# Kernel optimization log

Hardware: AMD Instinct MI355X
Metric: run time of the kernel (lower is better)

The kernel has to match this reference:

```python
import jax, jax.numpy as jnp
import numpy as np

N_NODES = 150000       # original nodes
N_FRAG_NODES = 300000  # nodes duplicated across fragments
N_FRAGS = 30000        # number of fragments (segments of fragments_batch)
E = 1200000            # edges in combined fragment graph
D = 128                # nhid


def seg_mean(x, seg, num):
    s = jax.ops.segment_sum(x, seg, num_segments=num)
    c = jax.ops.segment_sum(jnp.ones((x.shape[0], 1), x.dtype), seg, num_segments=num)
    return s / jnp.maximum(c, 1.0)


def setup_inputs() -> dict:
    key = jax.random.key(0)
    ks = jax.random.split(key, 8)
    x = jax.random.normal(ks[0], (N_NODES, D), dtype=jnp.float32)
    mapper = jax.random.randint(ks[1], (N_FRAG_NODES,), 0, N_NODES)
    batch = jnp.sort(jax.random.randint(ks[2], (N_FRAG_NODES,), 0, N_FRAGS))
    edge_index = jax.random.randint(ks[3], (2, E), 0, N_FRAG_NODES)
    W_u = jax.random.normal(ks[4], (D, D), dtype=jnp.float32) * 0.05
    b_u = jnp.zeros((D,), dtype=jnp.float32)
    W_gcn = jax.random.normal(ks[5], (D, D), dtype=jnp.float32) * 0.05
    b_gcn = jnp.zeros((D,), dtype=jnp.float32)
    return {
        "x": x,
        "fragments_nodes_mapper": mapper,
        "fragments_batch": batch,
        "edge_index": edge_index,
        "W_u": W_u,
        "b_u": b_u,
        "W_gcn": W_gcn,
        "b_gcn": b_gcn,
        "i": 0,
    }


def gcn_conv(x, edge_index, W, b, n):
    # PyG GCNConv: add self loops, symmetric normalization D^-1/2 (A+I) D^-1/2, then linear.
    xw = x @ W  # [n, D]
    loops = jnp.arange(n, dtype=edge_index.dtype)
    row = jnp.concatenate([edge_index[0], loops])  # source
    col = jnp.concatenate([edge_index[1], loops])  # target (aggregation index)
    deg = jax.ops.segment_sum(jnp.ones(row.shape[0], x.dtype), col, num_segments=n)
    dinv = jnp.where(deg > 0, jax.lax.rsqrt(jnp.maximum(deg, 1.0)), 0.0)
    norm = dinv[row] * dinv[col]  # [E+n]
    msg = xw[row] * norm[:, None]
    out = jax.ops.segment_sum(msg, col, num_segments=n)
    return out + b


def reference(x, fragments_nodes_mapper, fragments_batch, edge_index, W_u, b_u, W_gcn, b_gcn, i):
    if i == 0:
        x = x[fragments_nodes_mapper]  # gather: [N_FRAG_NODES, D]
    # fragment-level mean pooling, broadcast back to fragment-nodes
    fragment = seg_mean(x, fragments_batch, N_FRAGS)[fragments_batch]
    # U[i-1]: MLP(nhid, nhid, nlayer=1, with_final_activation=True) -> Linear + ReLU
    x = x + jax.nn.relu(fragment @ W_u + b_u)
    # pool duplicated fragment-nodes back onto original nodes, then re-broadcast
    x = seg_mean(x, fragments_nodes_mapper, N_NODES)[fragments_nodes_mapper]
    # GCN over the combined fragment graph
    x = gcn_conv(x, edge_index, W_gcn, b_gcn, N_FRAG_NODES)
    fragment_x = seg_mean(x, fragments_batch, N_FRAGS)  # [N_FRAGS, D]
    return (fragment_x, x)
```

## Files before the change

### kernel.cpp

```cpp
#include <hip/hip_runtime.h>
#include <hip/hip_bf16.h>

#define N_NODES      150000
#define N_FRAG_NODES 300000
#define N_FRAGS      30000
#define NEDGE        1200000
#define NCNT         (N_NODES + N_FRAG_NODES)
#define D            128
#define DV           32
#define SCAN_TILE    1024

typedef __attribute__((ext_vector_type(8))) short short8;
typedef __attribute__((ext_vector_type(8))) unsigned short u16x8;
typedef __attribute__((ext_vector_type(4))) float f32x4;

__device__ __forceinline__ unsigned short f2bf(float f) {
    unsigned u = __float_as_uint(f);
    u = (u + 0x7FFFu + ((u >> 16) & 1u)) >> 16;
    return (unsigned short)u;
}
__device__ __forceinline__ float bf2f(unsigned short u) {
    return __uint_as_float((unsigned)u << 16);
}

__global__ void k_prep(const int* __restrict__ mapper, const int* __restrict__ batch,
                       const int* __restrict__ ecol, int* __restrict__ mcnt,
                       int* __restrict__ ccnt, int* __restrict__ startb) {
    int i = blockIdx.x * blockDim.x + threadIdx.x;
    if (i < NEDGE) atomicAdd(&ccnt[ecol[i]], 1);
    if (i < N_FRAG_NODES) atomicAdd(&mcnt[mapper[i]], 1);
    if (i <= N_FRAGS) {
        int lo = 0, hi = N_FRAG_NODES;
        while (lo < hi) { int mid = (lo + hi) >> 1; if (batch[mid] < i) lo = mid + 1; else hi = mid; }
        startb[i] = lo;
    }
}

__global__ void k_scan_tile(const int* __restrict__ cnt, int* __restrict__ combst,
                            int* __restrict__ tsum) {
    __shared__ int buf[SCAN_TILE];
    int tid = threadIdx.x;
    int i = blockIdx.x * SCAN_TILE + tid;
    int v = (i < NCNT) ? cnt[i] : 0;
    buf[tid] = v;
    __syncthreads();
    for (int off = 1; off < SCAN_TILE; off <<= 1) {
        int t = (tid >= off) ? buf[tid - off] : 0;
        __syncthreads();
        buf[tid] += t;
        __syncthreads();
    }
    if (i < NCNT) combst[i] = buf[tid] - v;
    if (tid == SCAN_TILE - 1) tsum[blockIdx.x] = buf[tid];
}

__global__ void k_scan_tsum(int* __restrict__ tsum, int ntiles,
                            int* __restrict__ mstart, int* __restrict__ cstart) {
    __shared__ int buf[SCAN_TILE];
    int tid = threadIdx.x;
    int v = (tid < ntiles) ? tsum[tid] : 0;
    buf[tid] = v;
    __syncthreads();
    for (int off = 1; off < SCAN_TILE; off <<= 1) {
        int t = (tid >= off) ? buf[tid - off] : 0;
        __syncthreads();
        buf[tid] += t;
        __syncthreads();
    }
    if (tid < ntiles) tsum[tid] = buf[tid] - v;
    if (tid == SCAN_TILE - 1) {
        mstart[N_NODES] = N_FRAG_NODES;
        cstart[N_FRAG_NODES] = buf[tid] - N_FRAG_NODES;
    }
}

__global__ void k_scan_add(const int* __restrict__ combst, const int* __restrict__ tsum,
                           int* __restrict__ mstart, int* __restrict__ cstart) {
    int i = blockIdx.x * blockDim.x + threadIdx.x;
    if (i >= NCNT) return;
    int v = combst[i] + tsum[i >> 10];
    if (i < N_NODES) mstart[i] = v;
    else cstart[i - N_NODES] = v - N_FRAG_NODES;
}

__global__ void k_frag_mean(const float4* __restrict__ x4, const int* __restrict__ mapper,
                            const int* __restrict__ startb, ushort4* __restrict__ frag16) {
    int g = threadIdx.x >> 5, lane = threadIdx.x & 31;
    int b = blockIdx.x * 8 + g;
    if (b >= N_FRAGS) return;
    int s = startb[b], e = startb[b + 1];
    float4 sA = {0.f, 0.f, 0.f, 0.f}, sB = {0.f, 0.f, 0.f, 0.f};
    int j = s;
    for (; j + 2 <= e; j += 2) {
        int m0 = mapper[j], m1 = mapper[j + 1];
        float4 v0 = x4[(size_t)m0 * DV + lane];
        float4 v1 = x4[(size_t)m1 * DV + lane];
        sA.x += v0.x; sA.y += v0.y; sA.z += v0.z; sA.w += v0.w;
        sB.x += v1.x; sB.y += v1.y; sB.z += v1.z; sB.w += v1.w;
    }
    if (j < e) {
        int m0 = mapper[j];
        float4 v0 = x4[(size_t)m0 * DV + lane];
        sA.x += v0.x; sA.y += v0.y; sA.z += v0.z; sA.w += v0.w;
    }
    float c = (float)(e - s); if (c < 1.f) c = 1.f;
    float inv = 1.f / c;
    ushort4 r = {f2bf((sA.x + sB.x) * inv), f2bf((sA.y + sB.y) * inv),
                 f2bf((sA.z + sB.z) * inv), f2bf((sA.w + sB.w) * inv)};
    frag16[(size_t)b * DV + lane] = r;
}

__global__ void k_build_wfrag(const float* __restrict__ W, short* __restrict__ wfrag) {
    int t = threadIdx.x;
    for (int e = t; e < 2048; e += 256) {
        int nt = e >> 8;
        int kk = (e >> 6) & 3;
        int lane = e & 63;
        int col = nt * 16 + (lane & 15);
        int kb = kk * 32 + ((lane >> 4) << 3);
        short8 v;
        #pragma unroll
        for (int j = 0; j < 8; ++j) v[j] = (short)f2bf(W[(kb + j) * D + col]);
        ((short8*)wfrag)[e] = v;
    }
}

template <bool RELU, bool BIAS>
__global__ void __launch_bounds__(256)
k_rowmat_mfma(const unsigned short* __restrict__ src16, const short* __restrict__ wfrag,
              const float* __restrict__ bias, unsigned short* __restrict__ dst16, int rows) {
    __shared__ short8 wl[2048];
    int tid = threadIdx.x;
    for (int e = tid; e < 2048; e += 256) wl[e] = ((const short8*)wfrag)[e];
    __syncthreads();
    int wv = tid >> 6, lane = tid & 63;
    int lrow = lane & 15;
    int lk8 = (lane >> 4);
    float bv[8];
    #pragma unroll
    for (int nt = 0; nt < 8; ++nt) bv[nt] = BIAS ? bias[nt * 16 + lrow] : 0.f;

    int chunk = blockIdx.x * 64;
    {
        int r = chunk + wv * 16 + lrow;
        short8 af[4];
        if (r < rows) {
            const short8* rowp = (const short8*)(src16 + (size_t)r * D);
            #pragma unroll
            for (int kk = 0; kk < 4; ++kk) af[kk] = rowp[kk * 4 + lk8];
        } else {
            #pragma unroll
            for (int kk = 0; kk < 4; ++kk) af[kk] = (short8)0;
        }
        f32x4 acc[8];
        #pragma unroll
        for (int nt = 0; nt < 8; ++nt) acc[nt] = (f32x4)0.f;
        #pragma unroll
        for (int nt = 0; nt < 8; ++nt) {
            #pragma unroll
            for (int kk = 0; kk < 4; ++kk)
                acc[nt] = __builtin_amdgcn_mfma_f32_16x16x32_bf16(
                              af[kk], wl[(nt * 4 + kk) * 64 + lane], acc[nt], 0, 0, 0);
        }
        int orow0 = chunk + wv * 16 + ((lane >> 4) << 2);
        #pragma unroll
        for (int nt = 0; nt < 8; ++nt) {
            int col = nt * 16 + lrow;
            #pragma unroll
            for (int reg = 0; reg < 4; ++reg) {
                int orow = orow0 + reg;
                if (orow < rows) {
                    float v = acc[nt][reg] + bv[nt];
                    if (RELU) v = fmaxf(v, 0.f);
                    dst16[(size_t)orow * D + col] = f2bf(v);
                }
            }
        }
    }
}

__global__ void k_fill_m(const int* __restrict__ mapper, const int* __restrict__ batch,
                         const int* __restrict__ mstart, int* __restrict__ mcnt,
                         int* __restrict__ mvals) {
    int i = blockIdx.x * blockDim.x + threadIdx.x;
    if (i >= N_FRAG_NODES) return;
    int k = mapper[i];
    int pos = atomicSub(&mcnt[k], 1) - 1;
    mvals[mstart[k] + pos] = batch[i];
}

__global__ void k_fill_e(const int* __restrict__ erow, const int* __restrict__ ecol,
                         const int* __restrict__ mapper, const int* __restrict__ cstart,
                         int* __restrict__ ccnt, int2* __restrict__ erecs) {
    int i = blockIdx.x * blockDim.x + threadIdx.x;
    if (i >= NEDGE) return;
    int c = ecol[i], r = erow[i];
    int pos = atomicSub(&ccnt[c], 1) - 1;
    float w = rsqrtf((float)(cstart[r + 1] - cstart[r] + 1));
    int2 rec;
    rec.x = mapper[r];
    rec.y = __float_as_int(w);
    erecs[cstart[c] + pos] = rec;
}

__global__ void k_pool_csr(const float4* __restrict__ x4, const u16x8* __restrict__ fragu8,
                           const int* __restrict__ mstart, const int* __restrict__ mvals,
                           u16x8* __restrict__ pooled8) {
    int g = threadIdx.x >> 4, lane = threadIdx.x & 15;
    int n = blockIdx.x * 16 + g;
    if (n >= N_NODES) return;
    int s = mstart[n], e = mstart[n + 1];
    u16x8 out = (u16x8)0;
    if (e > s) {
        float accA[8], accB[8];
        #pragma unroll
        for (int j = 0; j < 8; ++j) { accA[j] = 0.f; accB[j] = 0.f; }
        int t = s;
        for (; t + 2 <= e; t += 2) {
            int b0 = mvals[t], b1 = mvals[t + 1];
            u16x8 u0 = fragu8[(size_t)b0 * 16 + lane];
            u16x8 u1 = fragu8[(size_t)b1 * 16 + lane];
            #pragma unroll
            for (int j = 0; j < 8; ++j) {
                accA[j] += bf2f(u0[j]);
                accB[j] += bf2f(u1[j]);
            }
        }
        if (t < e) {
            int b0 = mvals[t];
            u16x8 u0 = fragu8[(size_t)b0 * 16 + lane];
            #pragma unroll
            for (int j = 0; j < 8; ++j) accA[j] += bf2f(u0[j]);
        }
        float inv = 1.f / (float)(e - s);
        float4 xv0 = x4[(size_t)n * DV + lane * 2];
        float4 xv1 = x4[(size_t)n * DV + lane * 2 + 1];
        out[0] = f2bf(fmaf(accA[0] + accB[0], inv, xv0.x));
        out[1] = f2bf(fmaf(accA[1] + accB[1], inv, xv0.y));
        out[2] = f2bf(fmaf(accA[2] + accB[2], inv, xv0.z));
        out[3] = f2bf(fmaf(accA[3] + accB[3], inv, xv0.w));
        out[4] = f2bf(fmaf(accA[4] + accB[4], inv, xv1.x));
        out[5] = f2bf(fmaf(accA[5] + accB[5], inv, xv1.y));
        out[6] = f2bf(fmaf(accA[6] + accB[6], inv, xv1.z));
        out[7] = f2bf(fmaf(accA[7] + accB[7], inv, xv1.w));
    }
    pooled8[(size_t)n * 16 + lane] = out;
}

__global__ void k_gcn_gather(const int* __restrict__ mapper, const int* __restrict__ cstart,
                             const int2* __restrict__ erecs, const u16x8* __restrict__ pw8,
                             const float* __restrict__ bgcn, float4* __restrict__ xout4) {
    int g = threadIdx.x >> 4, lane = threadIdx.x & 15;
    int c = blockIdx.x * 16 + g;
    if (c >= N_FRAG_NODES) return;
    int s = cstart[c], e = cstart[c + 1];
    float dc = rsqrtf((float)(e - s + 1));
    float accA[8], accB[8];
    #pragma unroll
    for (int j = 0; j < 8; ++j) { accA[j] = 0.f; accB[j] = 0.f; }
    int t = s;
    for (; t + 2 <= e; t += 2) {
        int2 r0 = erecs[t];
        int2 r1 = erecs[t + 1];
        u16x8 u0 = pw8[(size_t)r0.x * 16 + lane];
        u16x8 u1 = pw8[(size_t)r1.x * 16 + lane];
        float w0 = __int_as_float(r0.y);
        float w1 = __int_as_float(r1.y);
        #pragma unroll
        for (int j = 0; j < 8; ++j) {
            accA[j] = fmaf(bf2f(u0[j]), w0, accA[j]);
            accB[j] = fmaf(bf2f(u1[j]), w1, accB[j]);
        }
    }
    if (t < e) {
        int2 r0 = erecs[t];
        u16x8 u0 = pw8[(size_t)r0.x * 16 + lane];
        float w0 = __int_as_float(r0.y);
        #pragma unroll
        for (int j = 0; j < 8; ++j) accA[j] = fmaf(bf2f(u0[j]), w0, accA[j]);
    }
    u16x8 su = pw8[(size_t)mapper[c] * 16 + lane];
    float dc2 = dc * dc;
    const float4* bg4 = (const float4*)bgcn;
    float4 b0 = bg4[lane * 2], b1 = bg4[lane * 2 + 1];
    float4 o0, o1;
    o0.x = fmaf(accA[0] + accB[0], dc, fmaf(bf2f(su[0]), dc2, b0.x));
    o0.y = fmaf(accA[1] + accB[1], dc, fmaf(bf2f(su[1]), dc2, b0.y));
    o0.z = fmaf(accA[2] + accB[2], dc, fmaf(bf2f(su[2]), dc2, b0.z));
    o0.w = fmaf(accA[3] + accB[3], dc, fmaf(bf2f(su[3]), dc2, b0.w));
    o1.x = fmaf(accA[4] + accB[4], dc, fmaf(bf2f(su[4]), dc2, b1.x));
    o1.y = fmaf(accA[5] + accB[5], dc, fmaf(bf2f(su[5]), dc2, b1.y));
    o1.z = fmaf(accA[6] + accB[6], dc, fmaf(bf2f(su[6]), dc2, b1.z));
    o1.w = fmaf(accA[7] + accB[7], dc, fmaf(bf2f(su[7]), dc2, b1.w));
    xout4[(size_t)c * DV + lane * 2] = o0;
    xout4[(size_t)c * DV + lane * 2 + 1] = o1;
}

__global__ void k_frag_x(const float4* __restrict__ x4, const int* __restrict__ startb,
                         float4* __restrict__ fout4) {
    int g = threadIdx.x >> 5, lane = threadIdx.x & 31;
    int b = blockIdx.x * 8 + g;
    if (b >= N_FRAGS) return;
    int s = startb[b], e = startb[b + 1];
    float4 sA = {0.f, 0.f, 0.f, 0.f}, sB = {0.f, 0.f, 0.f, 0.f};
    int j = s;
    for (; j + 2 <= e; j += 2) {
        float4 v0 = x4[(size_t)j * DV + lane];
        float4 v1 = x4[(size_t)(j + 1) * DV + lane];
        sA.x += v0.x; sA.y += v0.y; sA.z += v0.z; sA.w += v0.w;
        sB.x += v1.x; sB.y += v1.y; sB.z += v1.z; sB.w += v1.w;
    }
    if (j < e) {
        float4 v0 = x4[(size_t)j * DV + lane];
        sA.x += v0.x; sA.y += v0.y; sA.z += v0.z; sA.w += v0.w;
    }
    float4 r = {0.f, 0.f, 0.f, 0.f};
    if (e > s) {
        float inv = 1.f / (float)(e - s);
        r.x = (sA.x + sB.x) * inv; r.y = (sA.y + sB.y) * inv;
        r.z = (sA.z + sB.z) * inv; r.w = (sA.w + sB.w) * inv;
    }
    fout4[(size_t)b * DV + lane] = r;
}

extern "C" void kernel_launch(void* const* d_in, const int* in_sizes, int n_in,
                              void* d_out, int out_size, void* d_ws, size_t ws_size,
                              hipStream_t stream) {
    const float* x      = (const float*)d_in[0];
    const int*   mapper = (const int*)d_in[1];
    const int*   batch  = (const int*)d_in[2];
    const int*   erow   = (const int*)d_in[3];
    const int*   ecol   = erow + NEDGE;
    const float* W_u    = (const float*)d_in[4];
    const float* b_u    = (const float*)d_in[5];
    const float* W_gcn  = (const float*)d_in[6];
    const float* b_gcn  = (const float*)d_in[7];

    float* fout = (float*)d_out;
    float* xout = fout + (size_t)N_FRAGS * D;

    short*  wfragU   = (short*)d_ws;
    short*  wfragG   = wfragU + 16384;
    int2*   erecs    = (int2*)(wfragG + 16384);
    unsigned short* frag16   = (unsigned short*)(erecs + NEDGE);
    unsigned short* pooled16 = frag16 + (size_t)N_FRAGS * D;
    int*    startb = (int*)(pooled16 + (size_t)N_NODES * D);
    int*    mstart = startb + (N_FRAGS + 1);
    int*    cstart = mstart + (N_NODES + 1);
    int*    mcnt   = cstart + (N_FRAG_NODES + 1);
    int*    ccnt   = mcnt + N_NODES;
    int*    mvals  = ccnt + N_FRAG_NODES;
    int*    combst = mvals + N_FRAG_NODES;
    int*    tsum   = combst + NCNT;

    hipMemsetAsync(mcnt, 0, (size_t)NCNT * sizeof(int), stream);

    k_build_wfrag<<<1, 256, 0, stream>>>(W_u, wfragU);
    k_build_wfrag<<<1, 256, 0, stream>>>(W_gcn, wfragG);

    k_prep<<<(NEDGE + 255) / 256, 256, 0, stream>>>(mapper, batch, ecol, mcnt, ccnt, startb);

    int ntiles = (NCNT + SCAN_TILE - 1) / SCAN_TILE;
    k_scan_tile<<<ntiles, SCAN_TILE, 0, stream>>>(mcnt, combst, tsum);
    k_scan_tsum<<<1, SCAN_TILE, 0, stream>>>(tsum, ntiles, mstart, cstart);
    k_scan_add<<<(NCNT + 255) / 256, 256, 0, stream>>>(combst, tsum, mstart, cstart);

    k_frag_mean<<<(N_FRAGS + 7) / 8, 256, 0, stream>>>((const float4*)x, mapper, startb,
                                                       (ushort4*)frag16);
    k_rowmat_mfma<true, true><<<(N_FRAGS + 63) / 64, 256, 0, stream>>>(
        frag16, wfragU, b_u, frag16, N_FRAGS);

    k_fill_m<<<(N_FRAG_NODES + 255) / 256, 256, 0, stream>>>(mapper, batch, mstart, mcnt, mvals);
    k_pool_csr<<<(N_NODES + 15) / 16, 256, 0, stream>>>((const float4*)x, (const u16x8*)frag16,
                                                        mstart, mvals, (u16x8*)pooled16);
    k_rowmat_mfma<false, false><<<(N_NODES + 63) / 64, 256, 0, stream>>>(
        pooled16, wfragG, nullptr, pooled16, N_NODES);

    k_fill_e<<<(NEDGE + 255) / 256, 256, 0, stream>>>(erow, ecol, mapper, cstart, ccnt, erecs);

    k_gcn_gather<<<(N_FRAG_NODES + 15) / 16, 256, 0, stream>>>(mapper, cstart, erecs,
                                                               (const u16x8*)pooled16,
                                                               b_gcn, (float4*)xout);
    k_frag_x<<<(N_FRAGS + 7) / 8, 256, 0, stream>>>((const float4*)xout, startb, (float4*)fout);
}
```

Baseline: 366.9 us.

## Fuse GCN gather with fragment mean and merge CSR fill kernels

Merges the GCN gather and the final fragment mean pooling into one kernel where each 16-lane group walks all nodes of a fragment, accumulating the mean in registers instead of re-reading the fp32 output. The two CSR fill kernels are combined into one launch, and a per-node precompute of (mapper, dinv) lets edge records be copied directly. Non-temporal loads and stores are used for edge records and the output. The trade-off is far fewer parallel work units: 30000 fragments instead of 300000 nodes, with variable-length serial loops per group, which can cause load imbalance and lower occupancy.

```diff
diff --git a/kernel.cpp b/kernel.cpp
--- a/kernel.cpp
+++ b/kernel.cpp
@@ -13,6 +13,7 @@
 typedef __attribute__((ext_vector_type(8))) short short8;
 typedef __attribute__((ext_vector_type(8))) unsigned short u16x8;
 typedef __attribute__((ext_vector_type(4))) float f32x4;
+typedef __attribute__((ext_vector_type(2))) int i32x2;
 
 __device__ __forceinline__ unsigned short f2bf(float f) {
     unsigned u = __float_as_uint(f);
@@ -179,28 +180,33 @@
     }
 }
 
-__global__ void k_fill_m(const int* __restrict__ mapper, const int* __restrict__ batch,
-                         const int* __restrict__ mstart, int* __restrict__ mcnt,
-                         int* __restrict__ mvals) {
+__global__ void k_sval(const int* __restrict__ mapper, const int* __restrict__ cstart,
+                       int2* __restrict__ sval) {
+    int r = blockIdx.x * blockDim.x + threadIdx.x;
+    if (r >= N_FRAG_NODES) return;
+    int2 v;
+    v.x = mapper[r];
+    v.y = __float_as_int(rsqrtf((float)(cstart[r + 1] - cstart[r] + 1)));
+    sval[r] = v;
+}
+
+__global__ void k_fill(const int* __restrict__ mapper, const int* __restrict__ batch,
+                       const int* __restrict__ erow, const int* __restrict__ ecol,
+                       const int* __restrict__ mstart, int* __restrict__ mcnt,
+                       int* __restrict__ mvals, const int* __restrict__ cstart,
+                       int* __restrict__ ccnt, const int2* __restrict__ sval,
+                       int2* __restrict__ erecs) {
     int i = blockIdx.x * blockDim.x + threadIdx.x;
-    if (i >= N_FRAG_NODES) return;
-    int k = mapper[i];
-    int pos = atomicSub(&mcnt[k], 1) - 1;
-    mvals[mstart[k] + pos] = batch[i];
-}
-
-__global__ void k_fill_e(const int* __restrict__ erow, const int* __restrict__ ecol,
-                         const int* __restrict__ mapper, const int* __restrict__ cstart,
-                         int* __restrict__ ccnt, int2* __restrict__ erecs) {
-    int i = blockIdx.x * blockDim.x + threadIdx.x;
-    if (i >= NEDGE) return;
-    int c = ecol[i], r = erow[i];
-    int pos = atomicSub(&ccnt[c], 1) - 1;
-    float w = rsqrtf((float)(cstart[r + 1] - cstart[r] + 1));
-    int2 rec;
-    rec.x = mapper[r];
-    rec.y = __float_as_int(w);
-    erecs[cstart[c] + pos] = rec;
+    if (i < N_FRAG_NODES) {
+        int k = mapper[i];
+        int pos = atomicSub(&mcnt[k], 1) - 1;
+        mvals[mstart[k] + pos] = batch[i];
+    }
+    if (i < NEDGE) {
+        int c = ecol[i], r = erow[i];
+        int pos = atomicSub(&ccnt[c], 1) - 1;
+        erecs[cstart[c] + pos] = sval[r];
+    }
 }
 
 __global__ void k_pool_csr(const float4* __restrict__ x4, const u16x8* __restrict__ fragu8,
@@ -247,80 +253,69 @@
     pooled8[(size_t)n * 16 + lane] = out;
 }
 
-__global__ void k_gcn_gather(const int* __restrict__ mapper, const int* __restrict__ cstart,
-                             const int2* __restrict__ erecs, const u16x8* __restrict__ pw8,
-                             const float* __restrict__ bgcn, float4* __restrict__ xout4) {
+__global__ void k_gcn_frag(const int* __restrict__ startb, const int* __restrict__ cstart,
+                           const int2* __restrict__ sval, const i32x2* __restrict__ erecs,
+                           const u16x8* __restrict__ pw8, const float* __restrict__ bgcn,
+                           f32x4* __restrict__ xout4, float4* __restrict__ fout4) {
     int g = threadIdx.x >> 4, lane = threadIdx.x & 15;
-    int c = blockIdx.x * 16 + g;
-    if (c >= N_FRAG_NODES) return;
-    int s = cstart[c], e = cstart[c + 1];
-    float dc = rsqrtf((float)(e - s + 1));
-    float accA[8], accB[8];
+    int b = blockIdx.x * 16 + g;
+    if (b >= N_FRAGS) return;
+    int js = startb[b], je = startb[b + 1];
+    const float4* bg4 = (const float4*)bgcn;
+    float4 bgA = bg4[lane * 2], bgB = bg4[lane * 2 + 1];
+    float mA[8];
     #pragma unroll
-    for (int j = 0; j < 8; ++j) { accA[j] = 0.f; accB[j] = 0.f; }
-    int t = s;
-    for (; t + 2 <= e; t += 2) {
-        int2 r0 = erecs[t];
-        int2 r1 = erecs[t + 1];
-        u16x8 u0 = pw8[(size_t)r0.x * 16 + lane];
-        u16x8 u1 = pw8[(size_t)r1.x * 16 + lane];
-        float w0 = __int_as_float(r0.y);
-        float w1 = __int_as_float(r1.y);
+    for (int j = 0; j < 8; ++j) mA[j] = 0.f;
+    for (int c = js; c < je; ++c) {
+        int s = cstart[c], e = cstart[c + 1];
+        int2 sv = sval[c];
+        float dc = __int_as_float(sv.y);
+        float accA[8], accB[8];
+        #pragma unroll
+        for (int j = 0; j < 8; ++j) { accA[j] = 0.f; accB[j] = 0.f; }
+        int t = s;
+        for (; t + 2 <= e; t += 2) {
+            i32x2 r0 = __builtin_nontemporal_load(&erecs[t]);
+            i32x2 r1 = __builtin_nontemporal_load(&erecs[t + 1]);
+            u16x8 u0 = pw8[(size_t)r0.x * 16 + lane];
+            u16x8 u1 = pw8[(size_t)r1.x * 16 + lane];
+            float w0 = __int_as_float(r0.y), w1 = __int_as_float(r1.y);
+            #pragma unroll
+            for (int j = 0; j < 8; ++j) {
+                accA[j] = fmaf(bf2f(u0[j]), w0, accA[j]);
+                accB[j] = fmaf(bf2f(u1[j]), w1, accB[j]);
+            }
+        }
+        if (t < e) {
+            i32x2 r0 = __builtin_nontemporal_load(&erecs[t]);
+            u16x8 u0 = pw8[(size_t)r0.x * 16 + lane];
+            float w0 = __int_as_float(r0.y);
+            #pragma unroll
+            for (int j = 0; j < 8; ++j) accA[j] = fmaf(bf2f(u0[j]), w0, accA[j]);
+        }
+        u16x8 su = pw8[(size_t)sv.x * 16 + lane];
+        float dc2 = dc * dc;
+        float o[8];
         #pragma unroll
         for (int j = 0; j < 8; ++j) {
-            accA[j] = fmaf(bf2f(u0[j]), w0, accA[j]);
-            accB[j] = fmaf(bf2f(u1[j]), w1, accB[j]);
-        }
-    }
-    if (t < e) {
-        int2 r0 = erecs[t];
-        u16x8 u0 = pw8[(size_t)r0.x * 16 + lane];
-        float w0 = __int_as_float(r0.y);
-        #pragma unroll
-        for (int j = 0; j < 8; ++j) accA[j] = fmaf(bf2f(u0[j]), w0, accA[j]);
-    }
-    u16x8 su = pw8[(size_t)mapper[c] * 16 + lane];
-    float dc2 = dc * dc;
-    const float4* bg4 = (const float4*)bgcn;
-    float4 b0 = bg4[lane * 2], b1 = bg4[lane * 2 + 1];
-    float4 o0, o1;
-    o0.x = fmaf(accA[0] + accB[0], dc, fmaf(bf2f(su[0]), dc2, b0.x));
-    o0.y = fmaf(accA[1] + accB[1], dc, fmaf(bf2f(su[1]), dc2, b0.y));
-    o0.z = fmaf(accA[2] + accB[2], dc, fmaf(bf2f(su[2]), dc2, b0.z));
-    o0.w = fmaf(accA[3] + accB[3], dc, fmaf(bf2f(su[3]), dc2, b0.w));
-    o1.x = fmaf(accA[4] + accB[4], dc, fmaf(bf2f(su[4]), dc2, b1.x));
-    o1.y = fmaf(accA[5] + accB[5], dc, fmaf(bf2f(su[5]), dc2, b1.y));
-    o1.z = fmaf(accA[6] + accB[6], dc, fmaf(bf2f(su[6]), dc2, b1.z));
-    o1.w = fmaf(accA[7] + accB[7], dc, fmaf(bf2f(su[7]), dc2, b1.w));
-    xout4[(size_t)c * DV + lane * 2] = o0;
-    xout4[(size_t)c * DV + lane * 2 + 1] = o1;
-}
-
-__global__ void k_frag_x(const float4* __restrict__ x4, const int* __restrict__ startb,
-                         float4* __restrict__ fout4) {
-    int g = threadIdx.x >> 5, lane = threadIdx.x & 31;
-    int b = blockIdx.x * 8 + g;
-    if (b >= N_FRAGS) return;
-    int s = startb[b], e = startb[b + 1];
-    float4 sA = {0.f, 0.f, 0.f, 0.f}, sB = {0.f, 0.f, 0.f, 0.f};
-    int j = s;
-    for (; j + 2 <= e; j += 2) {
-        float4 v0 = x4[(size_t)j * DV + lane];
-        float4 v1 = x4[(size_t)(j + 1) * DV + lane];
-        sA.x += v0.x; sA.y += v0.y; sA.z += v0.z; sA.w += v0.w;
-        sB.x += v1.x; sB.y += v1.y; sB.z += v1.z; sB.w += v1.w;
-    }
-    if (j < e) {
-        float4 v0 = x4[(size_t)j * DV + lane];
-        sA.x += v0.x; sA.y += v0.y; sA.z += v0.z; sA.w += v0.w;
-    }
-    float4 r = {0.f, 0.f, 0.f, 0.f};
-    if (e > s) {
-        float inv = 1.f / (float)(e - s);
-        r.x = (sA.x + sB.x) * inv; r.y = (sA.y + sB.y) * inv;
-        r.z = (sA.z + sB.z) * inv; r.w = (sA.w + sB.w) * inv;
-    }
-    fout4[(size_t)b * DV + lane] = r;
+            o[j] = fmaf(accA[j] + accB[j], dc, bf2f(su[j]) * dc2);
+            mA[j] += o[j];
+        }
+        f32x4 o0 = {o[0] + bgA.x, o[1] + bgA.y, o[2] + bgA.z, o[3] + bgA.w};
+        f32x4 o1 = {o[4] + bgB.x, o[5] + bgB.y, o[6] + bgB.z, o[7] + bgB.w};
+        __builtin_nontemporal_store(o0, &xout4[(size_t)c * DV + lane * 2]);
+        __builtin_nontemporal_store(o1, &xout4[(size_t)c * DV + lane * 2 + 1]);
+    }
+    float4 r0 = {0.f, 0.f, 0.f, 0.f}, r1 = {0.f, 0.f, 0.f, 0.f};
+    if (je > js) {
+        float inv = 1.f / (float)(je - js);
+        r0.x = fmaf(mA[0], inv, bgA.x); r0.y = fmaf(mA[1], inv, bgA.y);
+        r0.z = fmaf(mA[2], inv, bgA.z); r0.w = fmaf(mA[3], inv, bgA.w);
+        r1.x = fmaf(mA[4], inv, bgB.x); r1.y = fmaf(mA[5], inv, bgB.y);
+        r1.z = fmaf(mA[6], inv, bgB.z); r1.w = fmaf(mA[7], inv, bgB.w);
+    }
+    fout4[(size_t)b * DV + lane * 2] = r0;
+    fout4[(size_t)b * DV + lane * 2 + 1] = r1;
 }
 
 extern "C" void kernel_launch(void* const* d_in, const int* in_sizes, int n_in,
@@ -342,7 +337,8 @@
     short*  wfragU   = (short*)d_ws;
     short*  wfragG   = wfragU + 16384;
     int2*   erecs    = (int2*)(wfragG + 16384);
-    unsigned short* frag16   = (unsigned short*)(erecs + NEDGE);
+    int2*   sval     = erecs + NEDGE;
+    unsigned short* frag16   = (unsigned short*)(sval + N_FRAG_NODES);
     unsigned short* pooled16 = frag16 + (size_t)N_FRAGS * D;
     int*    startb = (int*)(pooled16 + (size_t)N_NODES * D);
     int*    mstart = startb + (N_FRAGS + 1);
@@ -370,16 +366,17 @@
     k_rowmat_mfma<true, true><<<(N_FRAGS + 63) / 64, 256, 0, stream>>>(
         frag16, wfragU, b_u, frag16, N_FRAGS);
 
-    k_fill_m<<<(N_FRAG_NODES + 255) / 256, 256, 0, stream>>>(mapper, batch, mstart, mcnt, mvals);
+    k_sval<<<(N_FRAG_NODES + 255) / 256, 256, 0, stream>>>(mapper, cstart, sval);
+    k_fill<<<(NEDGE + 255) / 256, 256, 0, stream>>>(mapper, batch, erow, ecol,
+                                                    mstart, mcnt, mvals,
+                                                    cstart, ccnt, sval, erecs);
+
     k_pool_csr<<<(N_NODES + 15) / 16, 256, 0, stream>>>((const float4*)x, (const u16x8*)frag16,
                                                         mstart, mvals, (u16x8*)pooled16);
     k_rowmat_mfma<false, false><<<(N_NODES + 63) / 64, 256, 0, stream>>>(
         pooled16, wfragG, nullptr, pooled16, N_NODES);
 
-    k_fill_e<<<(NEDGE + 255) / 256, 256, 0, stream>>>(erow, ecol, mapper, cstart, ccnt, erecs);
-
-    k_gcn_gather<<<(N_FRAG_NODES + 15) / 16, 256, 0, stream>>>(mapper, cstart, erecs,
-                                                               (const u16x8*)pooled16,
-                                                               b_gcn, (float4*)xout);
-    k_frag_x<<<(N_FRAGS + 7) / 8, 256, 0, stream>>>((const float4*)xout, startb, (float4*)fout);
-}
+    k_gcn_frag<<<(N_FRAGS + 15) / 16, 256, 0, stream>>>(startb, cstart, sval, (const i32x2*)erecs,
+                                                        (const u16x8*)pooled16, b_gcn,
+                                                        (f32x4*)xout, (float4*)fout);
+}
```

After: 386.5 us. 1.05x slower.
